# Kernel tuning notes

Measured on AMD Instinct MI355X. Metric: run time of the kernel, lower is better.

## Reference

```python
import jax, jax.numpy as jnp
import numpy as np

# Config (from init_kwargs 'knn')
QUEUE_SIZE = 65536   # K
FEAT_DIM = 256       # D
BATCH = 512          # N (eval_sampling = 1.0 -> all samples used)
NUM_KNNS = 200
NUM_CLASSES = 1000
TEMPERATURE = 0.07


def _l2norm(x):
    return x / jnp.sqrt(jnp.sum(x * x, axis=-1, keepdims=True) + 1e-12)


def setup_inputs() -> dict:
    key = jax.random.key(0)
    k1, k2, k3, k4 = jax.random.split(key, 4)
    features = _l2norm(jax.random.normal(k1, (BATCH, FEAT_DIM), jnp.float32))
    labels = jax.random.randint(k2, (BATCH,), 0, NUM_CLASSES, jnp.int32)
    queue_features = _l2norm(jax.random.normal(k3, (QUEUE_SIZE, FEAT_DIM), jnp.float32))
    queue_labels = jax.random.randint(k4, (QUEUE_SIZE,), 0, NUM_CLASSES, jnp.int32)
    return {
        "features": features,
        "labels": labels,
        "queue_features": queue_features,
        "queue_labels": queue_labels,
        "queue_ptr": 0,
    }


def reference(features, labels, queue_features, queue_labels, queue_ptr):
    # ---- kNN accuracy (train branch, eval_sampling=1.0) ----
    sim = jnp.einsum('nc,kc->nk', features, queue_features)           # [N, K]
    sim_w, sim_idx = jax.lax.top_k(sim, k=NUM_KNNS)                   # [N, Kn]
    sim_w = jnp.exp(sim_w / TEMPERATURE)
    sim_labels = queue_labels[sim_idx]                                # [N, Kn] (vmapped gather)
    # weighted one-hot vote, expressed as a scatter-add (same math,
    # avoids the [N, Kn, C] one-hot intermediate)
    n = features.shape[0]
    pred_scores = jnp.zeros((n, NUM_CLASSES), sim_w.dtype)
    pred_scores = pred_scores.at[jnp.arange(n)[:, None], sim_labels].add(sim_w)
    pred_labels = jnp.argmax(pred_scores, axis=-1)
    accuracy = jnp.mean((pred_labels == labels).astype(jnp.float32))

    # ---- queue update (single device: all_gather == identity) ----
    batch_size = features.shape[0]
    inds = (jnp.arange(batch_size) + queue_ptr) % QUEUE_SIZE  # original asserts divisibility
    new_queue_features = queue_features.at[inds].set(features)
    new_queue_labels = queue_labels.at[inds].set(labels)
    new_queue_ptr = (queue_ptr + batch_size) % QUEUE_SIZE

    return accuracy, new_queue_features, new_queue_labels, new_queue_ptr
```

## Files before the change

kernel.cpp:

```cpp
#include <hip/hip_runtime.h>
#include <math.h>

#define NQ     65536
#define DIM    256
#define NBATCH 512
#define KNN    200
#define NCLS   1000
#define TSEL   0.14f

#define GM  128
#define GK  32
#define NTN (NQ / GM)

typedef unsigned short u16;
typedef unsigned long long u64;
typedef __attribute__((ext_vector_type(8))) short short8;
typedef __attribute__((ext_vector_type(4))) float f32x4;


__device__ __forceinline__ u16 f2bf(float x) {
  unsigned u = __float_as_uint(x);
  return (u16)((u + 0x7FFFu + ((u >> 16) & 1u)) >> 16);
}
__device__ __forceinline__ float bf2f(u16 h) {
  return __uint_as_float(((unsigned)h) << 16);
}
__device__ __forceinline__ void load_lds16(const void* g, void* l) {
  __builtin_amdgcn_global_load_lds(
      (const __attribute__((address_space(1))) unsigned int*)g,
      (__attribute__((address_space(3))) unsigned int*)l, 16, 0, 0);
}
__device__ __forceinline__ void store_f4u(float* p, float4 v) {
  p[0] = v.x;
  *(float2*)(p + 1) = make_float2(v.y, v.z);
  p[3] = v.w;
}

__global__ __launch_bounds__(256) void prep_copy_kernel(
    const float* __restrict__ feat, const int* __restrict__ labels,
    const float* __restrict__ qf, const int* __restrict__ ql,
    const int* __restrict__ qptr,
    u16* __restrict__ Bhi, u16* __restrict__ Blo,
    u16* __restrict__ Ahi, u16* __restrict__ Alo,
    int* __restrict__ flag, float* __restrict__ out)
{
  const int idx = blockIdx.x * 256 + threadIdx.x;
  const int ptr = qptr[0];
  const long long NFEAT = (long long)NQ * DIM;

  {
    float4 qv = ((const float4*)qf)[idx];
    int row = idx >> 6;
    int c4  = idx & 63;
    int d = (row - ptr) & (NQ - 1);
    float4 ov = qv;
    if (d < NBATCH) ov = ((const float4*)feat)[d * 64 + c4];
    store_f4u(out + 1 + 4 * (long long)idx, ov);

    ushort4 h, l;
    h.x = f2bf(qv.x); l.x = f2bf(qv.x - bf2f(h.x));
    h.y = f2bf(qv.y); l.y = f2bf(qv.y - bf2f(h.y));
    h.z = f2bf(qv.z); l.z = f2bf(qv.z - bf2f(h.z));
    h.w = f2bf(qv.w); l.w = f2bf(qv.w - bf2f(h.w));
    ((ushort4*)Bhi)[idx] = h;
    ((ushort4*)Blo)[idx] = l;
  }

  if (idx < NBATCH * DIM / 4) {
    float4 v = ((const float4*)feat)[idx];
    ushort4 h, l;
    h.x = f2bf(v.x); l.x = f2bf(v.x - bf2f(h.x));
    h.y = f2bf(v.y); l.y = f2bf(v.y - bf2f(h.y));
    h.z = f2bf(v.z); l.z = f2bf(v.z - bf2f(h.z));
    h.w = f2bf(v.w); l.w = f2bf(v.w - bf2f(h.w));
    ((ushort4*)Ahi)[idx] = h;
    ((ushort4*)Alo)[idx] = l;
  }

  if (idx < NQ) {
    int d = (idx - ptr) & (NQ - 1);
    int v = (d < NBATCH) ? labels[d] : ql[idx];
    out[1 + NFEAT + idx] = (float)v;
  }

  if (idx < NBATCH) flag[idx] = 0;
  if (idx == 0) {
    out[0] = 0.0f;
    out[1 + NFEAT + NQ] = (float)((ptr + NBATCH) & (NQ - 1));
  }
}

__global__ __launch_bounds__(256) void gemm_mfma(
    const u16* __restrict__ Ahi, const u16* __restrict__ Alo,
    const u16* __restrict__ Bhi, const u16* __restrict__ Blo,
    uint2* __restrict__ cand, int* __restrict__ cnt2,
    int* __restrict__ flag, int SLOT)
{
  __shared__ u16 sA[2][GM][GK];
  __shared__ u16 sB[2][GM][GK];
  __shared__ int lcnt[GM];

  const int tid  = threadIdx.x;
  const int wave = tid >> 6, lane = tid & 63;
  const int d  = blockIdx.x;
  const int bm = (d >> 3) & 3;
  const int bn = (d & 7) | ((d >> 5) << 3);

  for (int i = tid; i < GM; i += 256) lcnt[i] = 0;

  const u16* srcBase;
  u16* ldsBase;
  if (wave == 0)      { srcBase = Ahi + (size_t)bm * GM * DIM; ldsBase = &sA[0][0][0]; }
  else if (wave == 1) { srcBase = Alo + (size_t)bm * GM * DIM; ldsBase = &sA[1][0][0]; }
  else if (wave == 2) { srcBase = Bhi + (size_t)bn * GM * DIM; ldsBase = &sB[0][0][0]; }
  else                { srcBase = Blo + (size_t)bn * GM * DIM; ldsBase = &sB[1][0][0]; }
  const u16* src = srcBase + (lane >> 2) * DIM + (lane & 3) * 8;

  const int wm = (wave & 1) * 64, wn = (wave >> 1) * 64;
  const int fr = lane & 15;
  const int fq = lane >> 4;

  f32x4 acc[4][4] = {};

  for (int kk = 0; kk < DIM; kk += GK) {
    const u16* s = src + kk;
#pragma unroll
    for (int g = 0; g < 8; ++g)
      load_lds16(s + g * 16 * DIM, ldsBase + g * 512);
    __syncthreads();

    short8 ah[4], al[4], bh[4], bl[4];
#pragma unroll
    for (int i = 0; i < 4; ++i) {
      ah[i] = *(const short8*)&sA[0][wm + i * 16 + fr][fq * 8];
      al[i] = *(const short8*)&sA[1][wm + i * 16 + fr][fq * 8];
      bh[i] = *(const short8*)&sB[0][wn + i * 16 + fr][fq * 8];
      bl[i] = *(const short8*)&sB[1][wn + i * 16 + fr][fq * 8];
    }
#pragma unroll
    for (int i = 0; i < 4; ++i)
#pragma unroll
      for (int j = 0; j < 4; ++j) {
        acc[i][j] = __builtin_amdgcn_mfma_f32_16x16x32_bf16(ah[i], bh[j], acc[i][j], 0, 0, 0);
        acc[i][j] = __builtin_amdgcn_mfma_f32_16x16x32_bf16(ah[i], bl[j], acc[i][j], 0, 0, 0);
        acc[i][j] = __builtin_amdgcn_mfma_f32_16x16x32_bf16(al[i], bh[j], acc[i][j], 0, 0, 0);
      }
    __syncthreads();
  }

  const int lrow0 = wm + fq * 4;
  const int ccol  = bn * GM + wn + fr;
#pragma unroll
  for (int i = 0; i < 4; ++i)
#pragma unroll
    for (int j = 0; j < 4; ++j)
#pragma unroll
      for (int r = 0; r < 4; ++r) {
        float v = acc[i][j][r];
        if (v > TSEL) {
          int lr  = lrow0 + i * 16 + r;
          int col = ccol + j * 16;
          int p = atomicAdd(&lcnt[lr], 1);
          if (p < SLOT)
            cand[((size_t)(bm * GM + lr) * NTN + bn) * SLOT + p] =
                make_uint2(__float_as_uint(v), (unsigned)col);
          else
            flag[bm * GM + lr] = 1;
        }
      }
  __syncthreads();
  if (tid < GM) {
    int c = lcnt[tid];
    cnt2[(size_t)(bm * GM + tid) * NTN + bn] = c < SLOT ? c : SLOT;
  }
}

#define NBSEL 2048
#define CCAP  2048
#define MBCAP 256

__global__ __launch_bounds__(256) void select_kernel(
    const uint2* __restrict__ cand, const int* __restrict__ cnt2,
    const int* __restrict__ flag, const int* __restrict__ labels,
    const int* __restrict__ qlab, const float* __restrict__ qf,
    const float* __restrict__ feat, float* __restrict__ out,
    float inv_n, int SLOT)
{
  __shared__ int   hist[NBSEL];
  __shared__ int   seg[256];
  __shared__ float candV[CCAP];
  __shared__ int   candI[CCAP];
  __shared__ float votes[NCLS];
  __shared__ u64   bk[MBCAP];
  __shared__ float frow[DIM];
  __shared__ int   s_b, s_cnt, s_hi, s_mb;
  __shared__ u64   s_best;

  const int tid = threadIdx.x;
  const int row = blockIdx.x;

  bool fb = (flag[row] != 0);

  for (int i = tid; i < NBSEL; i += 256) hist[i] = 0;
  for (int c = tid; c < NCLS; c += 256) votes[c] = 0.0f;
  if (tid == 0) { s_b = 0; s_cnt = 0; s_hi = 0; s_mb = 0; s_best = 0ull; }
  __syncthreads();

  if (!fb) {
    const int*   rowcnt  = cnt2 + (size_t)row * NTN;
    const uint2* rowcand = cand + (size_t)row * NTN * SLOT;
    for (int t = tid; t < NTN; t += 256) {
      int c = rowcnt[t];
      if (c > 0) {
        int p = atomicAdd(&s_cnt, c);
        for (int k = 0; k < c; ++k) {
          if (p + k < CCAP) {
            uint2 e = rowcand[(size_t)t * SLOT + k];
            candV[p + k] = __uint_as_float(e.x);
            candI[p + k] = (int)e.y;
          }
        }
      }
    }
    __syncthreads();
    const int n = s_cnt;
    if (n < KNN || n > CCAP) fb = true;
    else {
      const float SSCALE = (float)NBSEL / (1.001f - TSEL);
      for (int i = tid; i < n; i += 256) {
        int b = (int)((candV[i] - TSEL) * SSCALE);
        b = b < 0 ? 0 : (b > NBSEL - 1 ? NBSEL - 1 : b);
        atomicAdd(&hist[b], 1);
      }
      __syncthreads();
      { int s = 0;
#pragma unroll
        for (int i = 0; i < 8; ++i) s += hist[tid * 8 + i];
        seg[tid] = s; }
      __syncthreads();
      for (int off = 1; off < 256; off <<= 1) {
        int t = (tid + off < 256) ? seg[tid + off] : 0;
        __syncthreads();
        seg[tid] += t;
        __syncthreads();
      }
      { int run = (tid < 255) ? seg[tid + 1] : 0;
        for (int i = tid * 8 + 7; i >= tid * 8; --i) {
          run += hist[i];
          if (run >= KNN) { atomicMax(&s_b, i); break; }
        } }
      __syncthreads();
      const int bstar = s_b;

      for (int i = tid; i < n; i += 256) {
        float v = candV[i];
        int b = (int)((v - TSEL) * SSCALE);
        b = b < 0 ? 0 : (b > NBSEL - 1 ? NBSEL - 1 : b);
        if (b > bstar) {
          atomicAdd(&s_hi, 1);
          atomicAdd(&votes[qlab[candI[i]]], expf(v * (1.0f / 0.07f)));
        } else if (b == bstar) {
          int p = atomicAdd(&s_mb, 1);
          if (p < MBCAP)
            bk[p] = ((u64)__float_as_uint(v) << 32) |
                    (u64)(0xFFFFFFFFu - (unsigned)candI[i]);
        }
      }
      __syncthreads();
      const int mb = s_mb;
      if (mb > MBCAP) fb = true;
      else {
        const int need = KNN - s_hi;
        for (int e = tid; e < mb; e += 256) {
          u64 ke = bk[e];
          int rank = 0;
          for (int j = 0; j < mb; ++j) rank += (bk[j] > ke);
          if (rank < need) {
            float v = __uint_as_float((unsigned)(ke >> 32));
            int col = (int)(0xFFFFFFFFu - (unsigned)(ke & 0xFFFFFFFFull));
            atomicAdd(&votes[qlab[col]], expf(v * (1.0f / 0.07f)));
          }
        }
        __syncthreads();
      }
    }
  }

  if (fb) {
    if (tid < DIM) frow[tid] = feat[(size_t)row * DIM + tid];
    for (int i = tid; i < NBSEL; i += 256) hist[i] = 0;
    if (tid == 0) { s_b = 0; s_cnt = 0; }
    __syncthreads();

    for (int q = tid; q < NQ; q += 256) {
      const float4* qr = (const float4*)(qf + (size_t)q * DIM);
      const float4* fr = (const float4*)frow;
      float s = 0.0f;
#pragma unroll
      for (int t = 0; t < DIM / 4; ++t) {
        float4 a = fr[t], b = qr[t];
        s = fmaf(a.x, b.x, s); s = fmaf(a.y, b.y, s);
        s = fmaf(a.z, b.z, s); s = fmaf(a.w, b.w, s);
      }
      int bin = (int)((s + 1.0f) * (NBSEL * 0.5f));
      bin = bin < 0 ? 0 : (bin > NBSEL - 1 ? NBSEL - 1 : bin);
      atomicAdd(&hist[bin], 1);
    }
    __syncthreads();

    { int s = 0;
#pragma unroll
      for (int i = 0; i < 8; ++i) s += hist[tid * 8 + i];
      seg[tid] = s; }
    __syncthreads();
    for (int off = 1; off < 256; off <<= 1) {
      int t = (tid + off < 256) ? seg[tid + off] : 0;
      __syncthreads();
      seg[tid] += t;
      __syncthreads();
    }
    { int run = (tid < 255) ? seg[tid + 1] : 0;
      for (int i = tid * 8 + 7; i >= tid * 8; --i) {
        run += hist[i];
        if (run >= KNN) { atomicMax(&s_b, i); break; }
      } }
    __syncthreads();
    const int bstar = s_b;

    for (int q = tid; q < NQ; q += 256) {
      const float4* qr = (const float4*)(qf + (size_t)q * DIM);
      const float4* fr = (const float4*)frow;
      float s = 0.0f;
#pragma unroll
      for (int t = 0; t < DIM / 4; ++t) {
        float4 a = fr[t], b = qr[t];
        s = fmaf(a.x, b.x, s); s = fmaf(a.y, b.y, s);
        s = fmaf(a.z, b.z, s); s = fmaf(a.w, b.w, s);
      }
      int bin = (int)((s + 1.0f) * (NBSEL * 0.5f));
      bin = bin < 0 ? 0 : (bin > NBSEL - 1 ? NBSEL - 1 : bin);
      if (bin >= bstar) {
        int p = atomicAdd(&s_cnt, 1);
        if (p < CCAP) { candV[p] = s; candI[p] = q; }
      }
    }
    __syncthreads();
    int m = s_cnt < CCAP ? s_cnt : CCAP;

    int P = 256; while (P < m) P <<= 1;
    for (int i = tid; i < P; i += 256)
      if (i >= m) { candV[i] = -INFINITY; candI[i] = 0x7fffffff; }
    __syncthreads();
    for (int k = 2; k <= P; k <<= 1) {
      for (int j = k >> 1; j > 0; j >>= 1) {
        for (int i = tid; i < P; i += 256) {
          int ixj = i ^ j;
          if (ixj > i) {
            float va = candV[i], vb = candV[ixj];
            int ia = candI[i], ib = candI[ixj];
            bool aFirst = (va > vb) || (va == vb && ia < ib);
            bool up = ((i & k) == 0);
            if (up ? !aFirst : aFirst) {
              candV[i] = vb; candV[ixj] = va;
              candI[i] = ib; candI[ixj] = ia;
            }
          }
        }
        __syncthreads();
      }
    }

    for (int c = tid; c < NCLS; c += 256) votes[c] = 0.0f;
    __syncthreads();
    for (int i = tid; i < KNN; i += 256)
      atomicAdd(&votes[qlab[candI[i]]], expf(candV[i] * (1.0f / 0.07f)));
    __syncthreads();
  }

  u64 key = 0ull;
  for (int c = tid; c < NCLS; c += 256) {
    u64 k2 = ((u64)__float_as_uint(votes[c]) << 32) |
             (u64)(0xFFFFFFFFu - (unsigned)c);
    if (k2 > key) key = k2;
  }
  for (int off = 32; off > 0; off >>= 1) {
    u64 o = __shfl_down(key, off, 64);
    if (o > key) key = o;
  }
  if ((tid & 63) == 0) atomicMax(&s_best, key);
  __syncthreads();
  if (tid == 0) {
    int cls = (int)(0xFFFFFFFFu - (unsigned)(s_best & 0xFFFFFFFFull));
    if (cls == labels[row]) atomicAdd(out, inv_n);
  }
}

extern "C" void kernel_launch(void* const* d_in, const int* in_sizes, int n_in,
                              void* d_out, int out_size, void* d_ws, size_t ws_size,
                              hipStream_t stream)
{
  const float* features = (const float*)d_in[0];
  const int*   labels   = (const int*)d_in[1];
  const float* qfeat    = (const float*)d_in[2];
  const int*   qlab     = (const int*)d_in[3];
  const int*   qptr     = (const int*)d_in[4];
  float* out = (float*)d_out;

  int nbatch = in_sizes[0] / DIM;
  float inv_n = 1.0f / (float)nbatch;

  size_t bBytes = (size_t)NQ * DIM * 2;
  size_t fixed  = 2 * bBytes + (size_t)NBATCH * NTN * 4 + NBATCH * 4 +
                  (size_t)NBATCH * DIM * 2 * 2;
  int SLOT = 16;
  while ((size_t)NBATCH * NTN * SLOT * 8 + fixed > ws_size && SLOT > 2) SLOT >>= 1;

  u16*   Bhi  = (u16*)d_ws;
  u16*   Blo  = Bhi + (size_t)NQ * DIM;
  uint2* cand = (uint2*)((char*)d_ws + 2 * bBytes);
  int*   cnt2 = (int*)((char*)cand + (size_t)NBATCH * NTN * SLOT * 8);
  int*   flagp = cnt2 + (size_t)NBATCH * NTN;
  u16*   Ahi  = (u16*)(flagp + NBATCH);
  u16*   Alo  = Ahi + (size_t)NBATCH * DIM;

  prep_copy_kernel<<<NQ * DIM / 4 / 256, 256, 0, stream>>>(
      features, labels, qfeat, qlab, qptr, Bhi, Blo, Ahi, Alo, flagp, out);

  gemm_mfma<<<(NBATCH / GM) * (NQ / GM), 256, 0, stream>>>(
      Ahi, Alo, Bhi, Blo, cand, cnt2, flagp, SLOT);

  select_kernel<<<nbatch, 256, 0, stream>>>(cand, cnt2, flagp, labels, qlab,
                                            qfeat, features, out, inv_n, SLOT);
}
```

Measured before the change: 244.5 us.

## Use single-bf16 GEMM for candidate filtering and rescore candidates in fp32

The split hi/lo bf16 GEMM (three MFMAs per tile) becomes a single bf16 pass that only filters candidates above a slightly higher threshold. Candidates are stored as column indices only, and the select kernel recomputes exact fp32 dot products for them before the histogram top-k. The GEMM also gets double-buffered LDS loads so the next K-slice is prefetched while the current one is computed. This cuts GEMM compute and workspace traffic in half or more. The cost is extra gather work in select, and a risk that bf16 error near the threshold drops true neighbours or overflows slots into the slow fallback.

New measurement: 216.0 us. 1.13x faster.

```diff
diff --git a/kernel.cpp b/kernel.cpp
--- a/kernel.cpp
+++ b/kernel.cpp
@@ -6,11 +6,13 @@
 #define NBATCH 512
 #define KNN    200
 #define NCLS   1000
-#define TSEL   0.14f
+#define TSELF  0.155f
+#define TSELH  0.150f
 
 #define GM  128
 #define GK  32
 #define NTN (NQ / GM)
+#define KSTEPS (DIM / GK)
 
 typedef unsigned short u16;
 typedef unsigned long long u64;
@@ -22,9 +24,6 @@
   unsigned u = __float_as_uint(x);
   return (u16)((u + 0x7FFFu + ((u >> 16) & 1u)) >> 16);
 }
-__device__ __forceinline__ float bf2f(u16 h) {
-  return __uint_as_float(((unsigned)h) << 16);
-}
 __device__ __forceinline__ void load_lds16(const void* g, void* l) {
   __builtin_amdgcn_global_load_lds(
       (const __attribute__((address_space(1))) unsigned int*)g,
@@ -40,8 +39,7 @@
     const float* __restrict__ feat, const int* __restrict__ labels,
     const float* __restrict__ qf, const int* __restrict__ ql,
     const int* __restrict__ qptr,
-    u16* __restrict__ Bhi, u16* __restrict__ Blo,
-    u16* __restrict__ Ahi, u16* __restrict__ Alo,
+    u16* __restrict__ Bb, u16* __restrict__ Ab,
     int* __restrict__ flag, float* __restrict__ out)
 {
   const int idx = blockIdx.x * 256 + threadIdx.x;
@@ -57,24 +55,16 @@
     if (d < NBATCH) ov = ((const float4*)feat)[d * 64 + c4];
     store_f4u(out + 1 + 4 * (long long)idx, ov);
 
-    ushort4 h, l;
-    h.x = f2bf(qv.x); l.x = f2bf(qv.x - bf2f(h.x));
-    h.y = f2bf(qv.y); l.y = f2bf(qv.y - bf2f(h.y));
-    h.z = f2bf(qv.z); l.z = f2bf(qv.z - bf2f(h.z));
-    h.w = f2bf(qv.w); l.w = f2bf(qv.w - bf2f(h.w));
-    ((ushort4*)Bhi)[idx] = h;
-    ((ushort4*)Blo)[idx] = l;
+    ushort4 h;
+    h.x = f2bf(qv.x); h.y = f2bf(qv.y); h.z = f2bf(qv.z); h.w = f2bf(qv.w);
+    ((ushort4*)Bb)[idx] = h;
   }
 
   if (idx < NBATCH * DIM / 4) {
     float4 v = ((const float4*)feat)[idx];
-    ushort4 h, l;
-    h.x = f2bf(v.x); l.x = f2bf(v.x - bf2f(h.x));
-    h.y = f2bf(v.y); l.y = f2bf(v.y - bf2f(h.y));
-    h.z = f2bf(v.z); l.z = f2bf(v.z - bf2f(h.z));
-    h.w = f2bf(v.w); l.w = f2bf(v.w - bf2f(h.w));
-    ((ushort4*)Ahi)[idx] = h;
-    ((ushort4*)Alo)[idx] = l;
+    ushort4 h;
+    h.x = f2bf(v.x); h.y = f2bf(v.y); h.z = f2bf(v.z); h.w = f2bf(v.w);
+    ((ushort4*)Ab)[idx] = h;
   }
 
   if (idx < NQ) {
@@ -91,9 +81,8 @@
 }
 
 __global__ __launch_bounds__(256) void gemm_mfma(
-    const u16* __restrict__ Ahi, const u16* __restrict__ Alo,
-    const u16* __restrict__ Bhi, const u16* __restrict__ Blo,
-    uint2* __restrict__ cand, int* __restrict__ cnt2,
+    const u16* __restrict__ A, const u16* __restrict__ B,
+    unsigned* __restrict__ cand, int* __restrict__ cnt2,
     int* __restrict__ flag, int SLOT)
 {
   __shared__ u16 sA[2][GM][GK];
@@ -108,13 +97,12 @@
 
   for (int i = tid; i < GM; i += 256) lcnt[i] = 0;
 
-  const u16* srcBase;
-  u16* ldsBase;
-  if (wave == 0)      { srcBase = Ahi + (size_t)bm * GM * DIM; ldsBase = &sA[0][0][0]; }
-  else if (wave == 1) { srcBase = Alo + (size_t)bm * GM * DIM; ldsBase = &sA[1][0][0]; }
-  else if (wave == 2) { srcBase = Bhi + (size_t)bn * GM * DIM; ldsBase = &sB[0][0][0]; }
-  else                { srcBase = Blo + (size_t)bn * GM * DIM; ldsBase = &sB[1][0][0]; }
+  const u16* srcBase = ((wave < 2) ? (A + (size_t)bm * GM * DIM)
+                                   : (B + (size_t)bn * GM * DIM))
+                       + (size_t)(wave & 1) * 64 * DIM;
   const u16* src = srcBase + (lane >> 2) * DIM + (lane & 3) * 8;
+  u16* dst0 = ((wave < 2) ? &sA[0][0][0] : &sB[0][0][0]) + (wave & 1) * 64 * GK;
+  u16* dst1 = ((wave < 2) ? &sA[1][0][0] : &sB[1][0][0]) + (wave & 1) * 64 * GK;
 
   const int wm = (wave & 1) * 64, wn = (wave >> 1) * 64;
   const int fr = lane & 15;
@@ -122,29 +110,36 @@
 
   f32x4 acc[4][4] = {};
 
-  for (int kk = 0; kk < DIM; kk += GK) {
-    const u16* s = src + kk;
-#pragma unroll
-    for (int g = 0; g < 8; ++g)
-      load_lds16(s + g * 16 * DIM, ldsBase + g * 512);
-    __syncthreads();
-
-    short8 ah[4], al[4], bh[4], bl[4];
+  {
+    const u16* s = src;
+#pragma unroll
+    for (int g = 0; g < 4; ++g)
+      load_lds16(s + g * 16 * DIM, dst0 + g * 512);
+  }
+  __syncthreads();
+
+  for (int t = 0; t < KSTEPS; ++t) {
+    const int cur = t & 1;
+    if (t + 1 < KSTEPS) {
+      const u16* s = src + (t + 1) * GK;
+      u16* dl = cur ? dst0 : dst1;
+#pragma unroll
+      for (int g = 0; g < 4; ++g)
+        load_lds16(s + g * 16 * DIM, dl + g * 512);
+    }
+
+    short8 a[4], b[4];
 #pragma unroll
     for (int i = 0; i < 4; ++i) {
-      ah[i] = *(const short8*)&sA[0][wm + i * 16 + fr][fq * 8];
-      al[i] = *(const short8*)&sA[1][wm + i * 16 + fr][fq * 8];
-      bh[i] = *(const short8*)&sB[0][wn + i * 16 + fr][fq * 8];
-      bl[i] = *(const short8*)&sB[1][wn + i * 16 + fr][fq * 8];
+      a[i] = *(const short8*)&sA[cur][wm + i * 16 + fr][fq * 8];
+      b[i] = *(const short8*)&sB[cur][wn + i * 16 + fr][fq * 8];
     }
 #pragma unroll
     for (int i = 0; i < 4; ++i)
 #pragma unroll
-      for (int j = 0; j < 4; ++j) {
-        acc[i][j] = __builtin_amdgcn_mfma_f32_16x16x32_bf16(ah[i], bh[j], acc[i][j], 0, 0, 0);
-        acc[i][j] = __builtin_amdgcn_mfma_f32_16x16x32_bf16(ah[i], bl[j], acc[i][j], 0, 0, 0);
-        acc[i][j] = __builtin_amdgcn_mfma_f32_16x16x32_bf16(al[i], bh[j], acc[i][j], 0, 0, 0);
-      }
+      for (int j = 0; j < 4; ++j)
+        acc[i][j] = __builtin_amdgcn_mfma_f32_16x16x32_bf16(a[i], b[j], acc[i][j], 0, 0, 0);
+
     __syncthreads();
   }
 
@@ -157,13 +152,12 @@
 #pragma unroll
       for (int r = 0; r < 4; ++r) {
         float v = acc[i][j][r];
-        if (v > TSEL) {
+        if (v > TSELF) {
           int lr  = lrow0 + i * 16 + r;
           int col = ccol + j * 16;
           int p = atomicAdd(&lcnt[lr], 1);
           if (p < SLOT)
-            cand[((size_t)(bm * GM + lr) * NTN + bn) * SLOT + p] =
-                make_uint2(__float_as_uint(v), (unsigned)col);
+            cand[((size_t)(bm * GM + lr) * NTN + bn) * SLOT + p] = (unsigned)col;
           else
             flag[bm * GM + lr] = 1;
         }
@@ -180,7 +174,7 @@
 #define MBCAP 256
 
 __global__ __launch_bounds__(256) void select_kernel(
-    const uint2* __restrict__ cand, const int* __restrict__ cnt2,
+    const unsigned* __restrict__ cand, const int* __restrict__ cnt2,
     const int* __restrict__ flag, const int* __restrict__ labels,
     const int* __restrict__ qlab, const float* __restrict__ qf,
     const float* __restrict__ feat, float* __restrict__ out,
@@ -201,34 +195,44 @@
 
   bool fb = (flag[row] != 0);
 
+  if (tid < DIM) frow[tid] = feat[(size_t)row * DIM + tid];
   for (int i = tid; i < NBSEL; i += 256) hist[i] = 0;
   for (int c = tid; c < NCLS; c += 256) votes[c] = 0.0f;
   if (tid == 0) { s_b = 0; s_cnt = 0; s_hi = 0; s_mb = 0; s_best = 0ull; }
   __syncthreads();
 
   if (!fb) {
-    const int*   rowcnt  = cnt2 + (size_t)row * NTN;
-    const uint2* rowcand = cand + (size_t)row * NTN * SLOT;
+    const int*      rowcnt  = cnt2 + (size_t)row * NTN;
+    const unsigned* rowcand = cand + (size_t)row * NTN * SLOT;
     for (int t = tid; t < NTN; t += 256) {
       int c = rowcnt[t];
       if (c > 0) {
         int p = atomicAdd(&s_cnt, c);
-        for (int k = 0; k < c; ++k) {
-          if (p + k < CCAP) {
-            uint2 e = rowcand[(size_t)t * SLOT + k];
-            candV[p + k] = __uint_as_float(e.x);
-            candI[p + k] = (int)e.y;
-          }
-        }
+        for (int k = 0; k < c; ++k)
+          if (p + k < CCAP) candI[p + k] = (int)rowcand[(size_t)t * SLOT + k];
       }
     }
     __syncthreads();
     const int n = s_cnt;
     if (n < KNN || n > CCAP) fb = true;
     else {
-      const float SSCALE = (float)NBSEL / (1.001f - TSEL);
+      const float4* fr4 = (const float4*)frow;
       for (int i = tid; i < n; i += 256) {
-        int b = (int)((candV[i] - TSEL) * SSCALE);
+        const float4* qr = (const float4*)(qf + (size_t)candI[i] * DIM);
+        float s = 0.0f;
+#pragma unroll 8
+        for (int t = 0; t < DIM / 4; ++t) {
+          float4 a = fr4[t], b = qr[t];
+          s = fmaf(a.x, b.x, s); s = fmaf(a.y, b.y, s);
+          s = fmaf(a.z, b.z, s); s = fmaf(a.w, b.w, s);
+        }
+        candV[i] = s;
+      }
+      __syncthreads();
+
+      const float SSCALE = (float)NBSEL / (1.001f - TSELH);
+      for (int i = tid; i < n; i += 256) {
+        int b = (int)((candV[i] - TSELH) * SSCALE);
         b = b < 0 ? 0 : (b > NBSEL - 1 ? NBSEL - 1 : b);
         atomicAdd(&hist[b], 1);
       }
@@ -254,7 +258,7 @@
 
       for (int i = tid; i < n; i += 256) {
         float v = candV[i];
-        int b = (int)((v - TSEL) * SSCALE);
+        int b = (int)((v - TSELH) * SSCALE);
         b = b < 0 ? 0 : (b > NBSEL - 1 ? NBSEL - 1 : b);
         if (b > bstar) {
           atomicAdd(&s_hi, 1);
@@ -287,7 +291,6 @@
   }
 
   if (fb) {
-    if (tid < DIM) frow[tid] = feat[(size_t)row * DIM + tid];
     for (int i = tid; i < NBSEL; i += 256) hist[i] = 0;
     if (tid == 0) { s_b = 0; s_cnt = 0; }
     __syncthreads();
@@ -410,24 +413,22 @@
   float inv_n = 1.0f / (float)nbatch;
 
   size_t bBytes = (size_t)NQ * DIM * 2;
-  size_t fixed  = 2 * bBytes + (size_t)NBATCH * NTN * 4 + NBATCH * 4 +
-                  (size_t)NBATCH * DIM * 2 * 2;
+  size_t fixed  = bBytes + (size_t)NBATCH * NTN * 4 + NBATCH * 4 +
+                  (size_t)NBATCH * DIM * 2;
   int SLOT = 16;
-  while ((size_t)NBATCH * NTN * SLOT * 8 + fixed > ws_size && SLOT > 2) SLOT >>= 1;
-
-  u16*   Bhi  = (u16*)d_ws;
-  u16*   Blo  = Bhi + (size_t)NQ * DIM;
-  uint2* cand = (uint2*)((char*)d_ws + 2 * bBytes);
-  int*   cnt2 = (int*)((char*)cand + (size_t)NBATCH * NTN * SLOT * 8);
-  int*   flagp = cnt2 + (size_t)NBATCH * NTN;
-  u16*   Ahi  = (u16*)(flagp + NBATCH);
-  u16*   Alo  = Ahi + (size_t)NBATCH * DIM;
+  while ((size_t)NBATCH * NTN * SLOT * 4 + fixed > ws_size && SLOT > 2) SLOT >>= 1;
+
+  u16*      Bb   = (u16*)d_ws;
+  unsigned* cand = (unsigned*)((char*)d_ws + bBytes);
+  int*      cnt2 = (int*)((char*)cand + (size_t)NBATCH * NTN * SLOT * 4);
+  int*      flagp = cnt2 + (size_t)NBATCH * NTN;
+  u16*      Ab   = (u16*)(flagp + NBATCH);
 
   prep_copy_kernel<<<NQ * DIM / 4 / 256, 256, 0, stream>>>(
-      features, labels, qfeat, qlab, qptr, Bhi, Blo, Ahi, Alo, flagp, out);
+      features, labels, qfeat, qlab, qptr, Bb, Ab, flagp, out);
 
   gemm_mfma<<<(NBATCH / GM) * (NQ / GM), 256, 0, stream>>>(
-      Ahi, Alo, Bhi, Blo, cand, cnt2, flagp, SLOT);
+      Ab, Bb, cand, cnt2, flagp, SLOT);
 
   select_kernel<<<nbatch, 256, 0, stream>>>(cand, cnt2, flagp, labels, qlab,
                                             qfeat, features, out, inv_n, SLOT);
```
